# Kernel tuning notes

Hardware: AMD Instinct MI355X
Metric: run time of the kernel (lower is better)

## Reference

```python
import jax, jax.numpy as jnp
import numpy as np
from jax import lax

B, T, IN, H = 4096, 512, 11, 16


def lstm(x, Wih, Whh, bih, bhh):
    # x: [B, T, in]; PyTorch gate order i, f, g, o packed along 4H.
    xg = jnp.einsum('bti,gi->btg', x, Wih) + bih + bhh  # [B, T, 4H]
    h0 = jnp.zeros((x.shape[0], Whh.shape[1]), x.dtype)
    c0 = jnp.zeros_like(h0)

    def step(carry, xg_t):
        h, c = carry
        g = xg_t + h @ Whh.T                      # [B, 4H]
        i, f, gg, o = jnp.split(g, 4, axis=-1)
        i = jax.nn.sigmoid(i)
        f = jax.nn.sigmoid(f)
        gg = jnp.tanh(gg)
        o = jax.nn.sigmoid(o)
        c = f * c + i * gg
        h = o * jnp.tanh(c)
        return (h, c), h

    _, hs = lax.scan(step, (h0, c0), jnp.swapaxes(xg, 0, 1))  # hs: [T, B, H]
    return jnp.swapaxes(hs, 0, 1)  # [B, T, H]


def setup_inputs() -> dict:
    key = jax.random.key(0)
    ks = jax.random.split(key, 16)
    s = 1.0 / np.sqrt(H)
    u = lambda k, shape: jax.random.uniform(k, shape, jnp.float32, -s, s)
    return {
        'x': jax.random.normal(ks[0], (B, T, IN), jnp.float32),
        'Wih1': u(ks[1], (4 * H, IN)), 'Whh1': u(ks[2], (4 * H, H)),
        'bih1': u(ks[3], (4 * H,)), 'bhh1': u(ks[4], (4 * H,)),
        'Wih2': u(ks[5], (4 * H, H)), 'Whh2': u(ks[6], (4 * H, H)),
        'bih2': u(ks[7], (4 * H,)), 'bhh2': u(ks[8], (4 * H,)),
        'Wd1': u(ks[9], (8, H)), 'bd1': u(ks[10], (8,)),
        'Wd2': u(ks[11], (8, 8)), 'bd2': u(ks[12], (8,)),
        'Wd3': u(ks[13], (3, 8)), 'bd3': u(ks[14], (3,)),
    }


def reference(x, Wih1, Whh1, bih1, bhh1, Wih2, Whh2, bih2, bhh2,
              Wd1, bd1, Wd2, bd2, Wd3, bd3):
    h1 = lstm(x, Wih1, Whh1, bih1, bhh1)          # [B, T, H]
    # Dropout2d treated as identity (eval mode).
    h2 = lstm(h1, Wih2, Whh2, bih2, bhh2)          # [B, T, H]
    s = jax.nn.softmax(h2, axis=1)[:, -1, :]       # softmax over TIME, take last step -> [B, H]
    d = (s @ Wd1.T + bd1) @ Wd2.T + bd2
    d = d @ Wd3.T + bd3                            # [B, 3]
    return jax.nn.softmax(d, axis=1)
```

## Files before the change

kernel.cpp:

```cpp
#include <hip/hip_runtime.h>

#define T_STEPS 512
#define IN_DIM 11
#define ROW_PAD 12
#define H_DIM 16
#define ROW_F (T_STEPS * IN_DIM)
#define CHUNK_T 16
#define CHUNK_F (CHUNK_T * IN_DIM)
#define N_CHUNK (T_STEPS / CHUNK_T)
#define LOG2E 1.44269504088896340736f

typedef float v2f __attribute__((ext_vector_type(2)));
typedef float v4f __attribute__((ext_vector_type(4)));

__device__ __forceinline__ v2f pk_fma(v2f a, v2f b, v2f c) {
    v2f d;
    asm("v_pk_fma_f32 %0, %1, %2, %3" : "=v"(d) : "v"(a), "v"(b), "v"(c));
    return d;
}

template<int CTRL>
__device__ __forceinline__ float qperm(float v) {
    return __builtin_bit_cast(float,
        __builtin_amdgcn_update_dpp(0, __builtin_bit_cast(int, v),
                                    CTRL, 0xf, 0xf, true));
}

__device__ __forceinline__ float bcast_lane(float v, int l) {
    return __builtin_bit_cast(float,
        __builtin_amdgcn_readlane(__builtin_bit_cast(int, v), l));
}

__global__ __launch_bounds__(256, 4) void lstm2_head(
    const float* __restrict__ x,
    const float* __restrict__ Wih1, const float* __restrict__ Whh1,
    const float* __restrict__ bih1, const float* __restrict__ bhh1,
    const float* __restrict__ Wih2, const float* __restrict__ Whh2,
    const float* __restrict__ bih2, const float* __restrict__ bhh2,
    const float* __restrict__ Wd1, const float* __restrict__ bd1,
    const float* __restrict__ Wd2, const float* __restrict__ bd2,
    const float* __restrict__ Wd3, const float* __restrict__ bd3,
    float* __restrict__ out)
{
    __shared__ float xlds[4][2][212];
    __shared__ alignas(16) v2f shh[4][2][8];

    const int lane = threadIdx.x & 63;
    const int wid = __builtin_amdgcn_readfirstlane((int)(threadIdx.x >> 6));
    const int b = blockIdx.x * 4 + wid;

    const int r   = lane >> 2;
    const int gt  = lane & 3;
    const int row = gt * H_DIM + r;

    const bool is_t = (gt == 2);
    const float M   = is_t ? (-2.0f * LOG2E) : (-LOG2E);
    const float vAa = is_t ? 2.0f : 1.0f;
    const float vBc = is_t ? -1.0f : 0.0f;

    v2f wi1p[6], wh1p[8], wi2p[8], wh2p[8];
    #pragma unroll
    for (int j = 0; j < 5; ++j)
        wi1p[j] = (v2f){M * Wih1[row * IN_DIM + 2 * j], M * Wih1[row * IN_DIM + 2 * j + 1]};
    wi1p[5] = (v2f){M * Wih1[row * IN_DIM + 10], 0.0f};
    #pragma unroll
    for (int j = 0; j < 8; ++j) {
        wh1p[j] = (v2f){M * Whh1[row * H_DIM + 2 * j], M * Whh1[row * H_DIM + 2 * j + 1]};
        wi2p[j] = (v2f){M * Wih2[row * H_DIM + 2 * j], M * Wih2[row * H_DIM + 2 * j + 1]};
        wh2p[j] = (v2f){M * Whh2[row * H_DIM + 2 * j], M * Whh2[row * H_DIM + 2 * j + 1]};
    }
    const float bb1 = M * (bih1[row] + bhh1[row]);
    const float bb2 = M * (bih2[row] + bhh2[row]);
    #pragma unroll
    for (int j = 0; j < 6; ++j) asm volatile("" : "+v"(wi1p[j]));
    #pragma unroll
    for (int j = 0; j < 8; ++j) {
        asm volatile("" : "+v"(wh1p[j]));
        asm volatile("" : "+v"(wi2p[j]));
        asm volatile("" : "+v"(wh2p[j]));
    }

    const float* __restrict__ xb = x + (size_t)b * ROW_F;
    float* const xl0 = &xlds[wid][0][0];
    float* const xl1 = &xlds[wid][1][0];
    v2f* const h1mem = &shh[wid][0][0];
    v2f* const h2mem = &shh[wid][1][0];
    const v4f* const h1q4 = (const v4f*)h1mem;
    const v4f* const h2q4 = (const v4f*)h2mem;

    ((float*)h1mem)[r & 15] = 0.0f;
    ((float*)h2mem)[r & 15] = 0.0f;
    if (lane < 32) {
        const int buf = lane >> 4, rr = lane & 15;
        xlds[wid][buf][rr * ROW_PAD + IN_DIM] = 0.0f;
    }

    const int f1i = lane, f2i = lane + 64, f3i = lane + 128;
    const int p1 = (f1i / IN_DIM) * ROW_PAD + (f1i % IN_DIM);
    const int p2 = (f2i / IN_DIM) * ROW_PAD + (f2i % IN_DIM);
    const int p3 = (f3i / IN_DIM) * ROW_PAD + (f3i % IN_DIM);

    float gl0 = xb[f1i];
    float gl1 = xb[f2i];
    float gl2 = xb[min(f3i, ROW_F - 1)];

    float c1 = 0.f, c2 = 0.f, h2v = 0.f, ssum = 0.f;
    v2f h1r[8], h2r[8];
    #pragma unroll
    for (int j = 0; j < 8; ++j) { h1r[j] = (v2f){0.f, 0.f}; h2r[j] = (v2f){0.f, 0.f}; }

    for (int ck = 0; ck < N_CHUNK; ++ck) {
        float* const xbuf = (ck & 1) ? xl1 : xl0;
        xbuf[p1] = gl0;
        xbuf[p2] = gl1;
        xbuf[p3] = gl2;
        if (ck + 1 < N_CHUNK) {
            const int base = (ck + 1) * CHUNK_F;
            gl0 = xb[base + f1i];
            gl1 = xb[base + f2i];
            gl2 = xb[min(base + f3i, ROW_F - 1)];
        }

        #pragma unroll
        for (int t2 = 0; t2 < CHUNK_T; ++t2) {
            const v2f* const xr = (const v2f*)(xbuf + t2 * ROW_PAD);

            v2f a2p = pk_fma(wh2p[0], h2r[0], (v2f){bb2, 0.f});
            v2f a2q = pk_fma(wh2p[1], h2r[1], (v2f){0.f, 0.f});
            #pragma unroll
            for (int j = 2; j < 8; j += 2) {
                a2p = pk_fma(wh2p[j],     h2r[j],     a2p);
                a2q = pk_fma(wh2p[j + 1], h2r[j + 1], a2q);
            }

            v2f a1p = pk_fma(wi1p[0], xr[0], (v2f){bb1, 0.f});
            v2f a1q = pk_fma(wi1p[1], xr[1], (v2f){0.f, 0.f});
            #pragma unroll
            for (int j = 2; j < 6; j += 2) {
                a1p = pk_fma(wi1p[j],     xr[j],     a1p);
                a1q = pk_fma(wi1p[j + 1], xr[j + 1], a1q);
            }
            #pragma unroll
            for (int j = 0; j < 8; j += 2) {
                a1p = pk_fma(wh1p[j],     h1r[j],     a1p);
                a1q = pk_fma(wh1p[j + 1], h1r[j + 1], a1q);
            }

            const v2f s1 = a1p + a1q;
            const float g1 = s1.x + s1.y;
            const float a1 = __builtin_fmaf(vAa,
                __builtin_amdgcn_rcpf(1.0f + __builtin_amdgcn_exp2f(g1)), vBc);
            {
                const float gi = qperm<0x00>(a1);
                const float gf = qperm<0x55>(a1);
                const float gg = qperm<0xAA>(a1);
                const float go = qperm<0xFF>(a1);
                c1 = __builtin_fmaf(gf, c1, gi * gg);
                const float tc = __builtin_fmaf(2.0f,
                    __builtin_amdgcn_rcpf(1.0f +
                        __builtin_amdgcn_exp2f(-2.0f * LOG2E * c1)), -1.0f);
                ((float*)h1mem)[r] = go * tc;
            }
            #pragma unroll
            for (int j = 0; j < 4; ++j) {
                const v4f q = h1q4[j];
                h1r[2 * j]     = (v2f){q.x, q.y};
                h1r[2 * j + 1] = (v2f){q.z, q.w};
            }

            #pragma unroll
            for (int j = 0; j < 8; j += 2) {
                a2p = pk_fma(wi2p[j],     h1r[j],     a2p);
                a2q = pk_fma(wi2p[j + 1], h1r[j + 1], a2q);
            }

            const v2f s2 = a2p + a2q;
            const float g2 = s2.x + s2.y;
            const float a2 = __builtin_fmaf(vAa,
                __builtin_amdgcn_rcpf(1.0f + __builtin_amdgcn_exp2f(g2)), vBc);
            {
                const float gi = qperm<0x00>(a2);
                const float gf = qperm<0x55>(a2);
                const float gg = qperm<0xAA>(a2);
                const float go = qperm<0xFF>(a2);
                c2 = __builtin_fmaf(gf, c2, gi * gg);
                const float tc = __builtin_fmaf(2.0f,
                    __builtin_amdgcn_rcpf(1.0f +
                        __builtin_amdgcn_exp2f(-2.0f * LOG2E * c2)), -1.0f);
                h2v = go * tc;
                ((float*)h2mem)[r] = h2v;
            }
            #pragma unroll
            for (int j = 0; j < 4; ++j) {
                const v4f q = h2q4[j];
                h2r[2 * j]     = (v2f){q.x, q.y};
                h2r[2 * j + 1] = (v2f){q.z, q.w};
            }

            ssum += __builtin_amdgcn_exp2f(LOG2E * h2v);
        }
    }

    const float sv = __builtin_amdgcn_exp2f(LOG2E * h2v) / ssum;

    float ssb[H_DIM];
    #pragma unroll
    for (int k = 0; k < H_DIM; ++k) ssb[k] = bcast_lane(sv, 4 * k);

    const int r8 = lane & 7;
    float acc1 = bd1[r8];
    #pragma unroll
    for (int k = 0; k < H_DIM; ++k)
        acc1 = __builtin_fmaf(Wd1[r8 * H_DIM + k], ssb[k], acc1);

    float d1s[8];
    #pragma unroll
    for (int j = 0; j < 8; ++j) d1s[j] = bcast_lane(acc1, j);

    float acc2 = bd2[r8];
    #pragma unroll
    for (int k = 0; k < 8; ++k)
        acc2 = __builtin_fmaf(Wd2[r8 * 8 + k], d1s[k], acc2);

    float d2s[8];
    #pragma unroll
    for (int j = 0; j < 8; ++j) d2s[j] = bcast_lane(acc2, j);

    float lg = 0.f;
    if (lane < 3) {
        lg = bd3[lane];
        #pragma unroll
        for (int k = 0; k < 8; ++k)
            lg = __builtin_fmaf(Wd3[lane * 8 + k], d2s[k], lg);
    }
    const float l0 = bcast_lane(lg, 0);
    const float l1 = bcast_lane(lg, 1);
    const float l2 = bcast_lane(lg, 2);
    const float mx = fmaxf(l0, fmaxf(l1, l2));
    const float e0 = __builtin_amdgcn_exp2f(LOG2E * (l0 - mx));
    const float e1 = __builtin_amdgcn_exp2f(LOG2E * (l1 - mx));
    const float e2 = __builtin_amdgcn_exp2f(LOG2E * (l2 - mx));
    const float inv = 1.0f / (e0 + e1 + e2);
    if (lane < 3) {
        const float ev = (lane == 0) ? e0 : ((lane == 1) ? e1 : e2);
        out[b * 3 + lane] = ev * inv;
    }
}

extern "C" void kernel_launch(void* const* d_in, const int* in_sizes, int n_in,
                              void* d_out, int out_size, void* d_ws, size_t ws_size,
                              hipStream_t stream) {
    (void)in_sizes; (void)n_in; (void)out_size; (void)d_ws; (void)ws_size;
    const float* x    = (const float*)d_in[0];
    const float* Wih1 = (const float*)d_in[1];
    const float* Whh1 = (const float*)d_in[2];
    const float* bih1 = (const float*)d_in[3];
    const float* bhh1 = (const float*)d_in[4];
    const float* Wih2 = (const float*)d_in[5];
    const float* Whh2 = (const float*)d_in[6];
    const float* bih2 = (const float*)d_in[7];
    const float* bhh2 = (const float*)d_in[8];
    const float* Wd1  = (const float*)d_in[9];
    const float* bd1  = (const float*)d_in[10];
    const float* Wd2  = (const float*)d_in[11];
    const float* bd2  = (const float*)d_in[12];
    const float* Wd3  = (const float*)d_in[13];
    const float* bd3  = (const float*)d_in[14];

    lstm2_head<<<dim3(4096 / 4), dim3(256), 0, stream>>>(
        x, Wih1, Whh1, bih1, bhh1, Wih2, Whh2, bih2, bhh2,
        Wd1, bd1, Wd2, bd2, Wd3, bd3, (float*)d_out);
}
```

Before: 462.4 us.

## Split LSTM layers across specialized waves with a chunked h1 ring buffer

Each block now handles two sequences with four waves. Two waves run layer 1 and write h1 into a double-buffered LDS ring per 16-step chunk. The other two waves run layer 2 one chunk behind, and the waves hand off through a block barrier per chunk. This shortens each wave's per-step serial dependency chain to a single LSTM cell and doubles the number of resident waves, raising the occupancy hint to 8 blocks. The cost is a __syncthreads every chunk, one extra chunk of pipeline fill, and waves that sit idle during the first and last chunk.

Result: slower. 851.7 us (+84.2%).

```diff
diff --git a/kernel.cpp b/kernel.cpp
--- a/kernel.cpp
+++ b/kernel.cpp
@@ -31,7 +31,7 @@
         __builtin_amdgcn_readlane(__builtin_bit_cast(int, v), l));
 }
 
-__global__ __launch_bounds__(256, 4) void lstm2_head(
+__global__ __launch_bounds__(256, 8) void lstm2_head(
     const float* __restrict__ x,
     const float* __restrict__ Wih1, const float* __restrict__ Whh1,
     const float* __restrict__ bih1, const float* __restrict__ bhh1,
@@ -42,12 +42,15 @@
     const float* __restrict__ Wd3, const float* __restrict__ bd3,
     float* __restrict__ out)
 {
-    __shared__ float xlds[4][2][212];
-    __shared__ alignas(16) v2f shh[4][2][8];
+    __shared__ alignas(16) float xlds[2][212];
+    __shared__ alignas(16) float ring[2][2][CHUNK_T][H_DIM];
+    __shared__ alignas(16) float shh2[2][H_DIM];
 
     const int lane = threadIdx.x & 63;
     const int wid = __builtin_amdgcn_readfirstlane((int)(threadIdx.x >> 6));
-    const int b = blockIdx.x * 4 + wid;
+    const int isL2 = wid >> 1;
+    const int bw   = wid & 1;
+    const int b    = blockIdx.x * 2 + bw;
 
     const int r   = lane >> 2;
     const int gt  = lane & 3;
@@ -58,192 +61,205 @@
     const float vAa = is_t ? 2.0f : 1.0f;
     const float vBc = is_t ? -1.0f : 0.0f;
 
-    v2f wi1p[6], wh1p[8], wi2p[8], wh2p[8];
-    #pragma unroll
-    for (int j = 0; j < 5; ++j)
-        wi1p[j] = (v2f){M * Wih1[row * IN_DIM + 2 * j], M * Wih1[row * IN_DIM + 2 * j + 1]};
-    wi1p[5] = (v2f){M * Wih1[row * IN_DIM + 10], 0.0f};
+    v2f win[8], wrec[8];
+    float bb;
+    if (!isL2) {
+        #pragma unroll
+        for (int j = 0; j < 5; ++j)
+            win[j] = (v2f){M * Wih1[row * IN_DIM + 2 * j],
+                           M * Wih1[row * IN_DIM + 2 * j + 1]};
+        win[5] = (v2f){M * Wih1[row * IN_DIM + 10], 0.0f};
+        win[6] = (v2f){0.f, 0.f};
+        win[7] = (v2f){0.f, 0.f};
+        #pragma unroll
+        for (int j = 0; j < 8; ++j)
+            wrec[j] = (v2f){M * Whh1[row * H_DIM + 2 * j],
+                            M * Whh1[row * H_DIM + 2 * j + 1]};
+        bb = M * (bih1[row] + bhh1[row]);
+    } else {
+        #pragma unroll
+        for (int j = 0; j < 8; ++j) {
+            win[j]  = (v2f){M * Wih2[row * H_DIM + 2 * j],
+                            M * Wih2[row * H_DIM + 2 * j + 1]};
+            wrec[j] = (v2f){M * Whh2[row * H_DIM + 2 * j],
+                            M * Whh2[row * H_DIM + 2 * j + 1]};
+        }
+        bb = M * (bih2[row] + bhh2[row]);
+    }
     #pragma unroll
     for (int j = 0; j < 8; ++j) {
-        wh1p[j] = (v2f){M * Whh1[row * H_DIM + 2 * j], M * Whh1[row * H_DIM + 2 * j + 1]};
-        wi2p[j] = (v2f){M * Wih2[row * H_DIM + 2 * j], M * Wih2[row * H_DIM + 2 * j + 1]};
-        wh2p[j] = (v2f){M * Whh2[row * H_DIM + 2 * j], M * Whh2[row * H_DIM + 2 * j + 1]};
-    }
-    const float bb1 = M * (bih1[row] + bhh1[row]);
-    const float bb2 = M * (bih2[row] + bhh2[row]);
-    #pragma unroll
-    for (int j = 0; j < 6; ++j) asm volatile("" : "+v"(wi1p[j]));
-    #pragma unroll
-    for (int j = 0; j < 8; ++j) {
-        asm volatile("" : "+v"(wh1p[j]));
-        asm volatile("" : "+v"(wi2p[j]));
-        asm volatile("" : "+v"(wh2p[j]));
-    }
-
-    const float* __restrict__ xb = x + (size_t)b * ROW_F;
-    float* const xl0 = &xlds[wid][0][0];
-    float* const xl1 = &xlds[wid][1][0];
-    v2f* const h1mem = &shh[wid][0][0];
-    v2f* const h2mem = &shh[wid][1][0];
-    const v4f* const h1q4 = (const v4f*)h1mem;
-    const v4f* const h2q4 = (const v4f*)h2mem;
-
-    ((float*)h1mem)[r & 15] = 0.0f;
-    ((float*)h2mem)[r & 15] = 0.0f;
-    if (lane < 32) {
-        const int buf = lane >> 4, rr = lane & 15;
-        xlds[wid][buf][rr * ROW_PAD + IN_DIM] = 0.0f;
+        asm volatile("" : "+v"(win[j]));
+        asm volatile("" : "+v"(wrec[j]));
     }
 
     const int f1i = lane, f2i = lane + 64, f3i = lane + 128;
     const int p1 = (f1i / IN_DIM) * ROW_PAD + (f1i % IN_DIM);
     const int p2 = (f2i / IN_DIM) * ROW_PAD + (f2i % IN_DIM);
     const int p3 = (f3i / IN_DIM) * ROW_PAD + (f3i % IN_DIM);
-
-    float gl0 = xb[f1i];
-    float gl1 = xb[f2i];
-    float gl2 = xb[min(f3i, ROW_F - 1)];
-
-    float c1 = 0.f, c2 = 0.f, h2v = 0.f, ssum = 0.f;
-    v2f h1r[8], h2r[8];
+    const float* __restrict__ xb = x + (size_t)b * ROW_F;
+
+    float gl0 = 0.f, gl1 = 0.f, gl2 = 0.f;
+    if (!isL2) {
+        if (lane < 16) xlds[bw][lane * ROW_PAD + IN_DIM] = 0.0f;
+        gl0 = xb[f1i];
+        gl1 = xb[f2i];
+        gl2 = xb[min(f3i, ROW_F - 1)];
+    }
+
+    float cst = 0.f, ssum = 0.f, h2v = 0.f;
+    v2f hr[8];
     #pragma unroll
-    for (int j = 0; j < 8; ++j) { h1r[j] = (v2f){0.f, 0.f}; h2r[j] = (v2f){0.f, 0.f}; }
-
-    for (int ck = 0; ck < N_CHUNK; ++ck) {
-        float* const xbuf = (ck & 1) ? xl1 : xl0;
-        xbuf[p1] = gl0;
-        xbuf[p2] = gl1;
-        xbuf[p3] = gl2;
-        if (ck + 1 < N_CHUNK) {
-            const int base = (ck + 1) * CHUNK_F;
-            gl0 = xb[base + f1i];
-            gl1 = xb[base + f2i];
-            gl2 = xb[min(base + f3i, ROW_F - 1)];
-        }
-
-        #pragma unroll
-        for (int t2 = 0; t2 < CHUNK_T; ++t2) {
-            const v2f* const xr = (const v2f*)(xbuf + t2 * ROW_PAD);
-
-            v2f a2p = pk_fma(wh2p[0], h2r[0], (v2f){bb2, 0.f});
-            v2f a2q = pk_fma(wh2p[1], h2r[1], (v2f){0.f, 0.f});
+    for (int j = 0; j < 8; ++j) hr[j] = (v2f){0.f, 0.f};
+
+    for (int ck = 0; ck <= N_CHUNK; ++ck) {
+        __syncthreads();
+
+        if (!isL2) {
+            if (ck < N_CHUNK) {
+                float* const xbuf = &xlds[bw][0];
+                xbuf[p1] = gl0;
+                xbuf[p2] = gl1;
+                xbuf[p3] = gl2;
+                if (ck + 1 < N_CHUNK) {
+                    const int base = (ck + 1) * CHUNK_F;
+                    gl0 = xb[base + f1i];
+                    gl1 = xb[base + f2i];
+                    gl2 = xb[min(base + f3i, ROW_F - 1)];
+                }
+                float (* const rg)[H_DIM] = ring[bw][ck & 1];
+                #pragma unroll
+                for (int t2 = 0; t2 < CHUNK_T; ++t2) {
+                    const v2f* const xr = (const v2f*)(xbuf + t2 * ROW_PAD);
+                    v2f ap = pk_fma(win[0], xr[0], (v2f){bb, 0.f});
+                    v2f aq = pk_fma(win[1], xr[1], (v2f){0.f, 0.f});
+                    ap = pk_fma(win[2], xr[2], ap);
+                    aq = pk_fma(win[3], xr[3], aq);
+                    ap = pk_fma(win[4], xr[4], ap);
+                    aq = pk_fma(win[5], xr[5], aq);
+                    #pragma unroll
+                    for (int j = 0; j < 8; j += 2) {
+                        ap = pk_fma(wrec[j],     hr[j],     ap);
+                        aq = pk_fma(wrec[j + 1], hr[j + 1], aq);
+                    }
+                    const v2f s = ap + aq;
+                    const float g = s.x + s.y;
+                    const float a = __builtin_fmaf(vAa,
+                        __builtin_amdgcn_rcpf(1.0f + __builtin_amdgcn_exp2f(g)), vBc);
+                    const float gi = qperm<0x00>(a);
+                    const float gf = qperm<0x55>(a);
+                    const float gg = qperm<0xAA>(a);
+                    const float go = qperm<0xFF>(a);
+                    cst = __builtin_fmaf(gf, cst, gi * gg);
+                    const float tc = __builtin_fmaf(2.0f,
+                        __builtin_amdgcn_rcpf(1.0f +
+                            __builtin_amdgcn_exp2f(-2.0f * LOG2E * cst)), -1.0f);
+                    rg[t2][r] = go * tc;
+                    const v4f* const hq = (const v4f*)&rg[t2][0];
+                    #pragma unroll
+                    for (int j = 0; j < 4; ++j) {
+                        const v4f q = hq[j];
+                        hr[2 * j]     = (v2f){q.x, q.y};
+                        hr[2 * j + 1] = (v2f){q.z, q.w};
+                    }
+                }
+            }
+        } else {
+            if (ck >= 1) {
+                float (* const rg)[H_DIM] = ring[bw][(ck - 1) & 1];
+                #pragma unroll
+                for (int t2 = 0; t2 < CHUNK_T; ++t2) {
+                    const v4f* const hq = (const v4f*)&rg[t2][0];
+                    const v4f q0 = hq[0];
+                    const v4f q1 = hq[1];
+                    v2f ap = pk_fma(wrec[0], hr[0], (v2f){bb, 0.f});
+                    v2f aq = pk_fma(wrec[1], hr[1], (v2f){0.f, 0.f});
+                    #pragma unroll
+                    for (int j = 2; j < 8; j += 2) {
+                        ap = pk_fma(wrec[j],     hr[j],     ap);
+                        aq = pk_fma(wrec[j + 1], hr[j + 1], aq);
+                    }
+                    ap = pk_fma(win[0], (v2f){q0.x, q0.y}, ap);
+                    aq = pk_fma(win[1], (v2f){q0.z, q0.w}, aq);
+                    const v4f q2 = hq[2];
+                    const v4f q3 = hq[3];
+                    ap = pk_fma(win[2], (v2f){q1.x, q1.y}, ap);
+                    aq = pk_fma(win[3], (v2f){q1.z, q1.w}, aq);
+                    ap = pk_fma(win[4], (v2f){q2.x, q2.y}, ap);
+                    aq = pk_fma(win[5], (v2f){q2.z, q2.w}, aq);
+                    ap = pk_fma(win[6], (v2f){q3.x, q3.y}, ap);
+                    aq = pk_fma(win[7], (v2f){q3.z, q3.w}, aq);
+                    const v2f s = ap + aq;
+                    const float g = s.x + s.y;
+                    const float a = __builtin_fmaf(vAa,
+                        __builtin_amdgcn_rcpf(1.0f + __builtin_amdgcn_exp2f(g)), vBc);
+                    const float gi = qperm<0x00>(a);
+                    const float gf = qperm<0x55>(a);
+                    const float gg = qperm<0xAA>(a);
+                    const float go = qperm<0xFF>(a);
+                    cst = __builtin_fmaf(gf, cst, gi * gg);
+                    const float tc = __builtin_fmaf(2.0f,
+                        __builtin_amdgcn_rcpf(1.0f +
+                            __builtin_amdgcn_exp2f(-2.0f * LOG2E * cst)), -1.0f);
+                    h2v = go * tc;
+                    shh2[bw][r] = h2v;
+                    const v4f* const h2q = (const v4f*)&shh2[bw][0];
+                    #pragma unroll
+                    for (int j = 0; j < 4; ++j) {
+                        const v4f q = h2q[j];
+                        hr[2 * j]     = (v2f){q.x, q.y};
+                        hr[2 * j + 1] = (v2f){q.z, q.w};
+                    }
+                    ssum += __builtin_amdgcn_exp2f(LOG2E * h2v);
+                }
+            }
+        }
+    }
+
+    if (isL2) {
+        const float sv = __builtin_amdgcn_exp2f(LOG2E * h2v) / ssum;
+
+        float ssb[H_DIM];
+        #pragma unroll
+        for (int k = 0; k < H_DIM; ++k) ssb[k] = bcast_lane(sv, 4 * k);
+
+        const int r8 = lane & 7;
+        float acc1 = bd1[r8];
+        #pragma unroll
+        for (int k = 0; k < H_DIM; ++k)
+            acc1 = __builtin_fmaf(Wd1[r8 * H_DIM + k], ssb[k], acc1);
+
+        float d1s[8];
+        #pragma unroll
+        for (int j = 0; j < 8; ++j) d1s[j] = bcast_lane(acc1, j);
+
+        float acc2 = bd2[r8];
+        #pragma unroll
+        for (int k = 0; k < 8; ++k)
+            acc2 = __builtin_fmaf(Wd2[r8 * 8 + k], d1s[k], acc2);
+
+        float d2s[8];
+        #pragma unroll
+        for (int j = 0; j < 8; ++j) d2s[j] = bcast_lane(acc2, j);
+
+        float lg = 0.f;
+        if (lane < 3) {
+            lg = bd3[lane];
             #pragma unroll
-            for (int j = 2; j < 8; j += 2) {
-                a2p = pk_fma(wh2p[j],     h2r[j],     a2p);
-                a2q = pk_fma(wh2p[j + 1], h2r[j + 1], a2q);
-            }
-
-            v2f a1p = pk_fma(wi1p[0], xr[0], (v2f){bb1, 0.f});
-            v2f a1q = pk_fma(wi1p[1], xr[1], (v2f){0.f, 0.f});
-            #pragma unroll
-            for (int j = 2; j < 6; j += 2) {
-                a1p = pk_fma(wi1p[j],     xr[j],     a1p);
-                a1q = pk_fma(wi1p[j + 1], xr[j + 1], a1q);
-            }
-            #pragma unroll
-            for (int j = 0; j < 8; j += 2) {
-                a1p = pk_fma(wh1p[j],     h1r[j],     a1p);
-                a1q = pk_fma(wh1p[j + 1], h1r[j + 1], a1q);
-            }
-
-            const v2f s1 = a1p + a1q;
-            const float g1 = s1.x + s1.y;
-            const float a1 = __builtin_fmaf(vAa,
-                __builtin_amdgcn_rcpf(1.0f + __builtin_amdgcn_exp2f(g1)), vBc);
-            {
-                const float gi = qperm<0x00>(a1);
-                const float gf = qperm<0x55>(a1);
-                const float gg = qperm<0xAA>(a1);
-                const float go = qperm<0xFF>(a1);
-                c1 = __builtin_fmaf(gf, c1, gi * gg);
-                const float tc = __builtin_fmaf(2.0f,
-                    __builtin_amdgcn_rcpf(1.0f +
-                        __builtin_amdgcn_exp2f(-2.0f * LOG2E * c1)), -1.0f);
-                ((float*)h1mem)[r] = go * tc;
-            }
-            #pragma unroll
-            for (int j = 0; j < 4; ++j) {
-                const v4f q = h1q4[j];
-                h1r[2 * j]     = (v2f){q.x, q.y};
-                h1r[2 * j + 1] = (v2f){q.z, q.w};
-            }
-
-            #pragma unroll
-            for (int j = 0; j < 8; j += 2) {
-                a2p = pk_fma(wi2p[j],     h1r[j],     a2p);
-                a2q = pk_fma(wi2p[j + 1], h1r[j + 1], a2q);
-            }
-
-            const v2f s2 = a2p + a2q;
-            const float g2 = s2.x + s2.y;
-            const float a2 = __builtin_fmaf(vAa,
-                __builtin_amdgcn_rcpf(1.0f + __builtin_amdgcn_exp2f(g2)), vBc);
-            {
-                const float gi = qperm<0x00>(a2);
-                const float gf = qperm<0x55>(a2);
-                const float gg = qperm<0xAA>(a2);
-                const float go = qperm<0xFF>(a2);
-                c2 = __builtin_fmaf(gf, c2, gi * gg);
-                const float tc = __builtin_fmaf(2.0f,
-                    __builtin_amdgcn_rcpf(1.0f +
-                        __builtin_amdgcn_exp2f(-2.0f * LOG2E * c2)), -1.0f);
-                h2v = go * tc;
-                ((float*)h2mem)[r] = h2v;
-            }
-            #pragma unroll
-            for (int j = 0; j < 4; ++j) {
-                const v4f q = h2q4[j];
-                h2r[2 * j]     = (v2f){q.x, q.y};
-                h2r[2 * j + 1] = (v2f){q.z, q.w};
-            }
-
-            ssum += __builtin_amdgcn_exp2f(LOG2E * h2v);
-        }
-    }
-
-    const float sv = __builtin_amdgcn_exp2f(LOG2E * h2v) / ssum;
-
-    float ssb[H_DIM];
-    #pragma unroll
-    for (int k = 0; k < H_DIM; ++k) ssb[k] = bcast_lane(sv, 4 * k);
-
-    const int r8 = lane & 7;
-    float acc1 = bd1[r8];
-    #pragma unroll
-    for (int k = 0; k < H_DIM; ++k)
-        acc1 = __builtin_fmaf(Wd1[r8 * H_DIM + k], ssb[k], acc1);
-
-    float d1s[8];
-    #pragma unroll
-    for (int j = 0; j < 8; ++j) d1s[j] = bcast_lane(acc1, j);
-
-    float acc2 = bd2[r8];
-    #pragma unroll
-    for (int k = 0; k < 8; ++k)
-        acc2 = __builtin_fmaf(Wd2[r8 * 8 + k], d1s[k], acc2);
-
-    float d2s[8];
-    #pragma unroll
-    for (int j = 0; j < 8; ++j) d2s[j] = bcast_lane(acc2, j);
-
-    float lg = 0.f;
-    if (lane < 3) {
-        lg = bd3[lane];
-        #pragma unroll
-        for (int k = 0; k < 8; ++k)
-            lg = __builtin_fmaf(Wd3[lane * 8 + k], d2s[k], lg);
-    }
-    const float l0 = bcast_lane(lg, 0);
-    const float l1 = bcast_lane(lg, 1);
-    const float l2 = bcast_lane(lg, 2);
-    const float mx = fmaxf(l0, fmaxf(l1, l2));
-    const float e0 = __builtin_amdgcn_exp2f(LOG2E * (l0 - mx));
-    const float e1 = __builtin_amdgcn_exp2f(LOG2E * (l1 - mx));
-    const float e2 = __builtin_amdgcn_exp2f(LOG2E * (l2 - mx));
-    const float inv = 1.0f / (e0 + e1 + e2);
-    if (lane < 3) {
-        const float ev = (lane == 0) ? e0 : ((lane == 1) ? e1 : e2);
-        out[b * 3 + lane] = ev * inv;
+            for (int k = 0; k < 8; ++k)
+                lg = __builtin_fmaf(Wd3[lane * 8 + k], d2s[k], lg);
+        }
+        const float l0 = bcast_lane(lg, 0);
+        const float l1 = bcast_lane(lg, 1);
+        const float l2 = bcast_lane(lg, 2);
+        const float mx = fmaxf(l0, fmaxf(l1, l2));
+        const float e0 = __builtin_amdgcn_exp2f(LOG2E * (l0 - mx));
+        const float e1 = __builtin_amdgcn_exp2f(LOG2E * (l1 - mx));
+        const float e2 = __builtin_amdgcn_exp2f(LOG2E * (l2 - mx));
+        const float inv = 1.0f / (e0 + e1 + e2);
+        if (lane < 3) {
+            const float ev = (lane == 0) ? e0 : ((lane == 1) ? e1 : e2);
+            out[b * 3 + lane] = ev * inv;
+        }
     }
 }
 
@@ -267,7 +283,7 @@
     const float* Wd3  = (const float*)d_in[13];
     const float* bd3  = (const float*)d_in[14];
 
-    lstm2_head<<<dim3(4096 / 4), dim3(256), 0, stream>>>(
+    lstm2_head<<<dim3(4096 / 2), dim3(256), 0, stream>>>(
         x, Wih1, Whh1, bih1, bhh1, Wih2, Whh2, bih2, bhh2,
         Wd1, bd1, Wd2, bd2, Wd3, bd3, (float*)d_out);
 }
```

## Split LSTM gate matvec across quad lanes with DPP transpose-reduce

Applied to the files above, without the earlier changes.

Previously each lane computed a full 16-wide dot product (plus 11 input terms) for its own gate row and reloaded the whole hidden vector from LDS. Now each lane in a quad handles a 4-element slice of k for all four gate rows of its hidden unit. Partial sums are exchanged with quad DPP permutes, so each lane reads only a 4-float slice of h and x. This shortens the serial FMA chain and LDS read volume per step on the recurrence critical path, at the cost of extra DPP adds and a wider padded x row layout.

New measurement: 473.1 us. 2.3% more time.

```diff
diff --git a/kernel.cpp b/kernel.cpp
--- a/kernel.cpp
+++ b/kernel.cpp
@@ -2,7 +2,7 @@
 
 #define T_STEPS 512
 #define IN_DIM 11
-#define ROW_PAD 12
+#define ROW_PAD 16
 #define H_DIM 16
 #define ROW_F (T_STEPS * IN_DIM)
 #define CHUNK_T 16
@@ -30,6 +30,21 @@
     return __builtin_bit_cast(float,
         __builtin_amdgcn_readlane(__builtin_bit_cast(int, v), l));
 }
+
+#define ACT_STEP(gsum, cst, hv_out)                                           \
+    {                                                                         \
+        const float a_ = __builtin_fmaf(vAa,                                  \
+            __builtin_amdgcn_rcpf(1.0f + __builtin_amdgcn_exp2f(gsum)), vBc); \
+        const float gi_ = qperm<0x00>(a_);                                    \
+        const float gf_ = qperm<0x55>(a_);                                    \
+        const float gg_ = qperm<0xAA>(a_);                                    \
+        const float go_ = qperm<0xFF>(a_);                                    \
+        cst = __builtin_fmaf(gf_, cst, gi_ * gg_);                            \
+        const float tc_ = __builtin_fmaf(2.0f,                                \
+            __builtin_amdgcn_rcpf(1.0f +                                      \
+                __builtin_amdgcn_exp2f(-2.0f * LOG2E * cst)), -1.0f);         \
+        hv_out = go_ * tc_;                                                   \
+    }
 
 __global__ __launch_bounds__(256, 4) void lstm2_head(
     const float* __restrict__ x,
@@ -42,8 +57,8 @@
     const float* __restrict__ Wd3, const float* __restrict__ bd3,
     float* __restrict__ out)
 {
-    __shared__ float xlds[4][2][212];
-    __shared__ alignas(16) v2f shh[4][2][8];
+    __shared__ alignas(16) float xlds[4][2][CHUNK_T * ROW_PAD];
+    __shared__ alignas(16) float shh[4][2][H_DIM];
 
     const int lane = threadIdx.x & 63;
     const int wid = __builtin_amdgcn_readfirstlane((int)(threadIdx.x >> 6));
@@ -54,45 +69,52 @@
     const int row = gt * H_DIM + r;
 
     const bool is_t = (gt == 2);
-    const float M   = is_t ? (-2.0f * LOG2E) : (-LOG2E);
     const float vAa = is_t ? 2.0f : 1.0f;
     const float vBc = is_t ? -1.0f : 0.0f;
-
-    v2f wi1p[6], wh1p[8], wi2p[8], wh2p[8];
-    #pragma unroll
-    for (int j = 0; j < 5; ++j)
-        wi1p[j] = (v2f){M * Wih1[row * IN_DIM + 2 * j], M * Wih1[row * IN_DIM + 2 * j + 1]};
-    wi1p[5] = (v2f){M * Wih1[row * IN_DIM + 10], 0.0f};
-    #pragma unroll
-    for (int j = 0; j < 8; ++j) {
-        wh1p[j] = (v2f){M * Whh1[row * H_DIM + 2 * j], M * Whh1[row * H_DIM + 2 * j + 1]};
-        wi2p[j] = (v2f){M * Wih2[row * H_DIM + 2 * j], M * Wih2[row * H_DIM + 2 * j + 1]};
-        wh2p[j] = (v2f){M * Whh2[row * H_DIM + 2 * j], M * Whh2[row * H_DIM + 2 * j + 1]};
-    }
-    const float bb1 = M * (bih1[row] + bhh1[row]);
-    const float bb2 = M * (bih2[row] + bhh2[row]);
-    #pragma unroll
-    for (int j = 0; j < 6; ++j) asm volatile("" : "+v"(wi1p[j]));
-    #pragma unroll
-    for (int j = 0; j < 8; ++j) {
-        asm volatile("" : "+v"(wh1p[j]));
-        asm volatile("" : "+v"(wi2p[j]));
-        asm volatile("" : "+v"(wh2p[j]));
+    const float Mown = is_t ? (-2.0f * LOG2E) : (-LOG2E);
+
+    v2f w1h[4][2], w1x[4][2], w2h[4][2], w2i[4][2];
+    #pragma unroll
+    for (int j = 0; j < 4; ++j) {
+        const int gj = gt ^ j;
+        const float Mj = (gj == 2) ? (-2.0f * LOG2E) : (-LOG2E);
+        const int rowj = gj * H_DIM + r;
+        #pragma unroll
+        for (int i2 = 0; i2 < 2; ++i2) {
+            const int k0 = 4 * gt + 2 * i2, k1 = k0 + 1;
+            w1h[j][i2] = (v2f){Mj * Whh1[rowj * H_DIM + k0],
+                               Mj * Whh1[rowj * H_DIM + k1]};
+            w1x[j][i2] = (v2f){k0 < IN_DIM ? Mj * Wih1[rowj * IN_DIM + k0] : 0.f,
+                               k1 < IN_DIM ? Mj * Wih1[rowj * IN_DIM + k1] : 0.f};
+            w2h[j][i2] = (v2f){Mj * Whh2[rowj * H_DIM + k0],
+                               Mj * Whh2[rowj * H_DIM + k1]};
+            w2i[j][i2] = (v2f){Mj * Wih2[rowj * H_DIM + k0],
+                               Mj * Wih2[rowj * H_DIM + k1]};
+        }
+    }
+    const float bb1 = Mown * (bih1[row] + bhh1[row]);
+    const float bb2 = Mown * (bih2[row] + bhh2[row]);
+    #pragma unroll
+    for (int j = 0; j < 4; ++j) {
+        #pragma unroll
+        for (int i2 = 0; i2 < 2; ++i2) {
+            asm volatile("" : "+v"(w1h[j][i2]));
+            asm volatile("" : "+v"(w1x[j][i2]));
+            asm volatile("" : "+v"(w2h[j][i2]));
+            asm volatile("" : "+v"(w2i[j][i2]));
+        }
     }
 
     const float* __restrict__ xb = x + (size_t)b * ROW_F;
     float* const xl0 = &xlds[wid][0][0];
     float* const xl1 = &xlds[wid][1][0];
-    v2f* const h1mem = &shh[wid][0][0];
-    v2f* const h2mem = &shh[wid][1][0];
-    const v4f* const h1q4 = (const v4f*)h1mem;
-    const v4f* const h2q4 = (const v4f*)h2mem;
-
-    ((float*)h1mem)[r & 15] = 0.0f;
-    ((float*)h2mem)[r & 15] = 0.0f;
-    if (lane < 32) {
-        const int buf = lane >> 4, rr = lane & 15;
-        xlds[wid][buf][rr * ROW_PAD + IN_DIM] = 0.0f;
+    float* const hsl1 = &shh[wid][0][0];
+    float* const hsl2 = &shh[wid][1][0];
+
+    #pragma unroll
+    for (int idx = 0; idx < CHUNK_T * ROW_PAD; idx += 64) {
+        const int s = idx + lane;
+        if ((s & 15) >= IN_DIM) { xl0[s] = 0.f; xl1[s] = 0.f; }
     }
 
     const int f1i = lane, f2i = lane + 64, f3i = lane + 128;
@@ -105,9 +127,10 @@
     float gl2 = xb[min(f3i, ROW_F - 1)];
 
     float c1 = 0.f, c2 = 0.f, h2v = 0.f, ssum = 0.f;
-    v2f h1r[8], h2r[8];
-    #pragma unroll
-    for (int j = 0; j < 8; ++j) { h1r[j] = (v2f){0.f, 0.f}; h2r[j] = (v2f){0.f, 0.f}; }
+    v2f h1a = (v2f){0.f, 0.f}, h1b = (v2f){0.f, 0.f};
+    v2f h2a = (v2f){0.f, 0.f}, h2b = (v2f){0.f, 0.f};
+
+    const int xoff = 4 * gt;
 
     for (int ck = 0; ck < N_CHUNK; ++ck) {
         float* const xbuf = (ck & 1) ? xl1 : xl0;
@@ -123,79 +146,68 @@
 
         #pragma unroll
         for (int t2 = 0; t2 < CHUNK_T; ++t2) {
-            const v2f* const xr = (const v2f*)(xbuf + t2 * ROW_PAD);
-
-            v2f a2p = pk_fma(wh2p[0], h2r[0], (v2f){bb2, 0.f});
-            v2f a2q = pk_fma(wh2p[1], h2r[1], (v2f){0.f, 0.f});
-            #pragma unroll
-            for (int j = 2; j < 8; j += 2) {
-                a2p = pk_fma(wh2p[j],     h2r[j],     a2p);
-                a2q = pk_fma(wh2p[j + 1], h2r[j + 1], a2q);
-            }
-
-            v2f a1p = pk_fma(wi1p[0], xr[0], (v2f){bb1, 0.f});
-            v2f a1q = pk_fma(wi1p[1], xr[1], (v2f){0.f, 0.f});
-            #pragma unroll
-            for (int j = 2; j < 6; j += 2) {
-                a1p = pk_fma(wi1p[j],     xr[j],     a1p);
-                a1q = pk_fma(wi1p[j + 1], xr[j + 1], a1q);
-            }
-            #pragma unroll
-            for (int j = 0; j < 8; j += 2) {
-                a1p = pk_fma(wh1p[j],     h1r[j],     a1p);
-                a1q = pk_fma(wh1p[j + 1], h1r[j + 1], a1q);
-            }
-
-            const v2f s1 = a1p + a1q;
-            const float g1 = s1.x + s1.y;
-            const float a1 = __builtin_fmaf(vAa,
-                __builtin_amdgcn_rcpf(1.0f + __builtin_amdgcn_exp2f(g1)), vBc);
-            {
-                const float gi = qperm<0x00>(a1);
-                const float gf = qperm<0x55>(a1);
-                const float gg = qperm<0xAA>(a1);
-                const float go = qperm<0xFF>(a1);
-                c1 = __builtin_fmaf(gf, c1, gi * gg);
-                const float tc = __builtin_fmaf(2.0f,
-                    __builtin_amdgcn_rcpf(1.0f +
-                        __builtin_amdgcn_exp2f(-2.0f * LOG2E * c1)), -1.0f);
-                ((float*)h1mem)[r] = go * tc;
-            }
-            #pragma unroll
-            for (int j = 0; j < 4; ++j) {
-                const v4f q = h1q4[j];
-                h1r[2 * j]     = (v2f){q.x, q.y};
-                h1r[2 * j + 1] = (v2f){q.z, q.w};
-            }
-
-            #pragma unroll
-            for (int j = 0; j < 8; j += 2) {
-                a2p = pk_fma(wi2p[j],     h1r[j],     a2p);
-                a2q = pk_fma(wi2p[j + 1], h1r[j + 1], a2q);
-            }
-
-            const v2f s2 = a2p + a2q;
-            const float g2 = s2.x + s2.y;
-            const float a2 = __builtin_fmaf(vAa,
-                __builtin_amdgcn_rcpf(1.0f + __builtin_amdgcn_exp2f(g2)), vBc);
-            {
-                const float gi = qperm<0x00>(a2);
-                const float gf = qperm<0x55>(a2);
-                const float gg = qperm<0xAA>(a2);
-                const float go = qperm<0xFF>(a2);
-                c2 = __builtin_fmaf(gf, c2, gi * gg);
-                const float tc = __builtin_fmaf(2.0f,
-                    __builtin_amdgcn_rcpf(1.0f +
-                        __builtin_amdgcn_exp2f(-2.0f * LOG2E * c2)), -1.0f);
-                h2v = go * tc;
-                ((float*)h2mem)[r] = h2v;
-            }
-            #pragma unroll
-            for (int j = 0; j < 4; ++j) {
-                const v4f q = h2q4[j];
-                h2r[2 * j]     = (v2f){q.x, q.y};
-                h2r[2 * j + 1] = (v2f){q.z, q.w};
-            }
+            const v4f xq = *(const v4f*)(xbuf + t2 * ROW_PAD + xoff);
+            const v2f x01 = (v2f){xq.x, xq.y};
+            const v2f x23 = (v2f){xq.z, xq.w};
+
+            v2f d0 = pk_fma(w1h[0][0], h1a, (v2f){bb1, 0.f});
+            d0 = pk_fma(w1h[0][1], h1b, d0);
+            d0 = pk_fma(w1x[0][0], x01, d0);
+            d0 = pk_fma(w1x[0][1], x23, d0);
+            v2f d1 = pk_fma(w1h[1][0], h1a, (v2f){0.f, 0.f});
+            d1 = pk_fma(w1h[1][1], h1b, d1);
+            d1 = pk_fma(w1x[1][0], x01, d1);
+            d1 = pk_fma(w1x[1][1], x23, d1);
+            v2f d2 = pk_fma(w1h[2][0], h1a, (v2f){0.f, 0.f});
+            d2 = pk_fma(w1h[2][1], h1b, d2);
+            d2 = pk_fma(w1x[2][0], x01, d2);
+            d2 = pk_fma(w1x[2][1], x23, d2);
+            v2f d3 = pk_fma(w1h[3][0], h1a, (v2f){0.f, 0.f});
+            d3 = pk_fma(w1h[3][1], h1b, d3);
+            d3 = pk_fma(w1x[3][0], x01, d3);
+            d3 = pk_fma(w1x[3][1], x23, d3);
+            const float u0 = d0.x + d0.y;
+            const float u1 = d1.x + d1.y;
+            const float u2 = d2.x + d2.y;
+            const float u3 = d3.x + d3.y;
+            const float g1v = u0 + qperm<0xB1>(u1)
+                                 + qperm<0x4E>(u2) + qperm<0x1B>(u3);
+
+            float h1v;
+            ACT_STEP(g1v, c1, h1v);
+            hsl1[r] = h1v;
+            const v4f h1q = *(const v4f*)(hsl1 + xoff);
+            h1a = (v2f){h1q.x, h1q.y};
+            h1b = (v2f){h1q.z, h1q.w};
+
+            v2f e0 = pk_fma(w2h[0][0], h2a, (v2f){bb2, 0.f});
+            e0 = pk_fma(w2h[0][1], h2b, e0);
+            e0 = pk_fma(w2i[0][0], h1a, e0);
+            e0 = pk_fma(w2i[0][1], h1b, e0);
+            v2f e1 = pk_fma(w2h[1][0], h2a, (v2f){0.f, 0.f});
+            e1 = pk_fma(w2h[1][1], h2b, e1);
+            e1 = pk_fma(w2i[1][0], h1a, e1);
+            e1 = pk_fma(w2i[1][1], h1b, e1);
+            v2f e2 = pk_fma(w2h[2][0], h2a, (v2f){0.f, 0.f});
+            e2 = pk_fma(w2h[2][1], h2b, e2);
+            e2 = pk_fma(w2i[2][0], h1a, e2);
+            e2 = pk_fma(w2i[2][1], h1b, e2);
+            v2f e3 = pk_fma(w2h[3][0], h2a, (v2f){0.f, 0.f});
+            e3 = pk_fma(w2h[3][1], h2b, e3);
+            e3 = pk_fma(w2i[3][0], h1a, e3);
+            e3 = pk_fma(w2i[3][1], h1b, e3);
+            const float v0 = e0.x + e0.y;
+            const float v1 = e1.x + e1.y;
+            const float v2 = e2.x + e2.y;
+            const float v3 = e3.x + e3.y;
+            const float g2v = v0 + qperm<0xB1>(v1)
+                                 + qperm<0x4E>(v2) + qperm<0x1B>(v3);
+
+            ACT_STEP(g2v, c2, h2v);
+            hsl2[r] = h2v;
+            const v4f h2q = *(const v4f*)(hsl2 + xoff);
+            h2a = (v2f){h2q.x, h2q.y};
+            h2b = (v2f){h2q.z, h2q.w};
 
             ssum += __builtin_amdgcn_exp2f(LOG2E * h2v);
         }
```

## Read x directly from global per step instead of staging chunks through LDS

Applied to the files above, without the earlier changes.

Removes the double-buffered LDS staging of input chunks and the chunk loop. Each timestep now loads its 11 input values straight from global memory (a uniform per-wave address, so effectively scalar or broadcast loads), computes the input projection with scalar FMAs, and folds it into the packed recurrent accumulator. The goal is to drop the LDS writes and reads and the chunk bookkeeping from the serial recurrence. The cost is global or cache load latency inside the dependent loop, which now relies on unroll-by-8 to hide it.

Measured after the change: 505.7 us. 1.09x slower.

```diff
diff --git a/kernel.cpp b/kernel.cpp
--- a/kernel.cpp
+++ b/kernel.cpp
@@ -2,12 +2,8 @@
 
 #define T_STEPS 512
 #define IN_DIM 11
-#define ROW_PAD 12
 #define H_DIM 16
 #define ROW_F (T_STEPS * IN_DIM)
-#define CHUNK_T 16
-#define CHUNK_F (CHUNK_T * IN_DIM)
-#define N_CHUNK (T_STEPS / CHUNK_T)
 #define LOG2E 1.44269504088896340736f
 
 typedef float v2f __attribute__((ext_vector_type(2)));
@@ -30,6 +26,21 @@
     return __builtin_bit_cast(float,
         __builtin_amdgcn_readlane(__builtin_bit_cast(int, v), l));
 }
+
+#define ACT_STEP(gsum, cst, hv_out)                                           \
+    {                                                                         \
+        const float a_ = __builtin_fmaf(vAa,                                  \
+            __builtin_amdgcn_rcpf(1.0f + __builtin_amdgcn_exp2f(gsum)), vBc); \
+        const float gi_ = qperm<0x00>(a_);                                    \
+        const float gf_ = qperm<0x55>(a_);                                    \
+        const float gg_ = qperm<0xAA>(a_);                                    \
+        const float go_ = qperm<0xFF>(a_);                                    \
+        cst = __builtin_fmaf(gf_, cst, gi_ * gg_);                            \
+        const float tc_ = __builtin_fmaf(2.0f,                                \
+            __builtin_amdgcn_rcpf(1.0f +                                      \
+                __builtin_amdgcn_exp2f(-2.0f * LOG2E * cst)), -1.0f);         \
+        hv_out = go_ * tc_;                                                   \
+    }
 
 __global__ __launch_bounds__(256, 4) void lstm2_head(
     const float* __restrict__ x,
@@ -42,8 +53,7 @@
     const float* __restrict__ Wd3, const float* __restrict__ bd3,
     float* __restrict__ out)
 {
-    __shared__ float xlds[4][2][212];
-    __shared__ alignas(16) v2f shh[4][2][8];
+    __shared__ alignas(16) float shh[4][2][H_DIM];
 
     const int lane = threadIdx.x & 63;
     const int wid = __builtin_amdgcn_readfirstlane((int)(threadIdx.x >> 6));
@@ -58,11 +68,10 @@
     const float vAa = is_t ? 2.0f : 1.0f;
     const float vBc = is_t ? -1.0f : 0.0f;
 
-    v2f wi1p[6], wh1p[8], wi2p[8], wh2p[8];
-    #pragma unroll
-    for (int j = 0; j < 5; ++j)
-        wi1p[j] = (v2f){M * Wih1[row * IN_DIM + 2 * j], M * Wih1[row * IN_DIM + 2 * j + 1]};
-    wi1p[5] = (v2f){M * Wih1[row * IN_DIM + 10], 0.0f};
+    float wx[IN_DIM];
+    #pragma unroll
+    for (int k = 0; k < IN_DIM; ++k) wx[k] = M * Wih1[row * IN_DIM + k];
+    v2f wh1p[8], wi2p[8], wh2p[8];
     #pragma unroll
     for (int j = 0; j < 8; ++j) {
         wh1p[j] = (v2f){M * Whh1[row * H_DIM + 2 * j], M * Whh1[row * H_DIM + 2 * j + 1]};
@@ -72,7 +81,7 @@
     const float bb1 = M * (bih1[row] + bhh1[row]);
     const float bb2 = M * (bih2[row] + bhh2[row]);
     #pragma unroll
-    for (int j = 0; j < 6; ++j) asm volatile("" : "+v"(wi1p[j]));
+    for (int k = 0; k < IN_DIM; ++k) asm volatile("" : "+v"(wx[k]));
     #pragma unroll
     for (int j = 0; j < 8; ++j) {
         asm volatile("" : "+v"(wh1p[j]));
@@ -80,125 +89,82 @@
         asm volatile("" : "+v"(wh2p[j]));
     }
 
+    float* const hs1 = &shh[wid][0][0];
+    float* const hs2 = &shh[wid][1][0];
+    const v4f* const h1q4 = (const v4f*)hs1;
+    const v4f* const h2q4 = (const v4f*)hs2;
+    hs1[r] = 0.0f;
+    hs2[r] = 0.0f;
+
     const float* __restrict__ xb = x + (size_t)b * ROW_F;
-    float* const xl0 = &xlds[wid][0][0];
-    float* const xl1 = &xlds[wid][1][0];
-    v2f* const h1mem = &shh[wid][0][0];
-    v2f* const h2mem = &shh[wid][1][0];
-    const v4f* const h1q4 = (const v4f*)h1mem;
-    const v4f* const h2q4 = (const v4f*)h2mem;
-
-    ((float*)h1mem)[r & 15] = 0.0f;
-    ((float*)h2mem)[r & 15] = 0.0f;
-    if (lane < 32) {
-        const int buf = lane >> 4, rr = lane & 15;
-        xlds[wid][buf][rr * ROW_PAD + IN_DIM] = 0.0f;
-    }
-
-    const int f1i = lane, f2i = lane + 64, f3i = lane + 128;
-    const int p1 = (f1i / IN_DIM) * ROW_PAD + (f1i % IN_DIM);
-    const int p2 = (f2i / IN_DIM) * ROW_PAD + (f2i % IN_DIM);
-    const int p3 = (f3i / IN_DIM) * ROW_PAD + (f3i % IN_DIM);
-
-    float gl0 = xb[f1i];
-    float gl1 = xb[f2i];
-    float gl2 = xb[min(f3i, ROW_F - 1)];
 
     float c1 = 0.f, c2 = 0.f, h2v = 0.f, ssum = 0.f;
     v2f h1r[8], h2r[8];
     #pragma unroll
     for (int j = 0; j < 8; ++j) { h1r[j] = (v2f){0.f, 0.f}; h2r[j] = (v2f){0.f, 0.f}; }
 
-    for (int ck = 0; ck < N_CHUNK; ++ck) {
-        float* const xbuf = (ck & 1) ? xl1 : xl0;
-        xbuf[p1] = gl0;
-        xbuf[p2] = gl1;
-        xbuf[p3] = gl2;
-        if (ck + 1 < N_CHUNK) {
-            const int base = (ck + 1) * CHUNK_F;
-            gl0 = xb[base + f1i];
-            gl1 = xb[base + f2i];
-            gl2 = xb[min(base + f3i, ROW_F - 1)];
-        }
-
-        #pragma unroll
-        for (int t2 = 0; t2 < CHUNK_T; ++t2) {
-            const v2f* const xr = (const v2f*)(xbuf + t2 * ROW_PAD);
-
-            v2f a2p = pk_fma(wh2p[0], h2r[0], (v2f){bb2, 0.f});
-            v2f a2q = pk_fma(wh2p[1], h2r[1], (v2f){0.f, 0.f});
-            #pragma unroll
-            for (int j = 2; j < 8; j += 2) {
-                a2p = pk_fma(wh2p[j],     h2r[j],     a2p);
-                a2q = pk_fma(wh2p[j + 1], h2r[j + 1], a2q);
-            }
-
-            v2f a1p = pk_fma(wi1p[0], xr[0], (v2f){bb1, 0.f});
-            v2f a1q = pk_fma(wi1p[1], xr[1], (v2f){0.f, 0.f});
-            #pragma unroll
-            for (int j = 2; j < 6; j += 2) {
-                a1p = pk_fma(wi1p[j],     xr[j],     a1p);
-                a1q = pk_fma(wi1p[j + 1], xr[j + 1], a1q);
-            }
-            #pragma unroll
-            for (int j = 0; j < 8; j += 2) {
-                a1p = pk_fma(wh1p[j],     h1r[j],     a1p);
-                a1q = pk_fma(wh1p[j + 1], h1r[j + 1], a1q);
-            }
-
-            const v2f s1 = a1p + a1q;
-            const float g1 = s1.x + s1.y;
-            const float a1 = __builtin_fmaf(vAa,
-                __builtin_amdgcn_rcpf(1.0f + __builtin_amdgcn_exp2f(g1)), vBc);
-            {
-                const float gi = qperm<0x00>(a1);
-                const float gf = qperm<0x55>(a1);
-                const float gg = qperm<0xAA>(a1);
-                const float go = qperm<0xFF>(a1);
-                c1 = __builtin_fmaf(gf, c1, gi * gg);
-                const float tc = __builtin_fmaf(2.0f,
-                    __builtin_amdgcn_rcpf(1.0f +
-                        __builtin_amdgcn_exp2f(-2.0f * LOG2E * c1)), -1.0f);
-                ((float*)h1mem)[r] = go * tc;
-            }
-            #pragma unroll
-            for (int j = 0; j < 4; ++j) {
-                const v4f q = h1q4[j];
-                h1r[2 * j]     = (v2f){q.x, q.y};
-                h1r[2 * j + 1] = (v2f){q.z, q.w};
-            }
-
-            #pragma unroll
-            for (int j = 0; j < 8; j += 2) {
-                a2p = pk_fma(wi2p[j],     h1r[j],     a2p);
-                a2q = pk_fma(wi2p[j + 1], h1r[j + 1], a2q);
-            }
-
-            const v2f s2 = a2p + a2q;
-            const float g2 = s2.x + s2.y;
-            const float a2 = __builtin_fmaf(vAa,
-                __builtin_amdgcn_rcpf(1.0f + __builtin_amdgcn_exp2f(g2)), vBc);
-            {
-                const float gi = qperm<0x00>(a2);
-                const float gf = qperm<0x55>(a2);
-                const float gg = qperm<0xAA>(a2);
-                const float go = qperm<0xFF>(a2);
-                c2 = __builtin_fmaf(gf, c2, gi * gg);
-                const float tc = __builtin_fmaf(2.0f,
-                    __builtin_amdgcn_rcpf(1.0f +
-                        __builtin_amdgcn_exp2f(-2.0f * LOG2E * c2)), -1.0f);
-                h2v = go * tc;
-                ((float*)h2mem)[r] = h2v;
-            }
-            #pragma unroll
-            for (int j = 0; j < 4; ++j) {
-                const v4f q = h2q4[j];
-                h2r[2 * j]     = (v2f){q.x, q.y};
-                h2r[2 * j + 1] = (v2f){q.z, q.w};
-            }
-
-            ssum += __builtin_amdgcn_exp2f(LOG2E * h2v);
-        }
+    #pragma unroll 8
+    for (int t = 0; t < T_STEPS; ++t) {
+        const float* __restrict__ xr = xb + t * IN_DIM;
+
+        float xs0 = __builtin_fmaf(wx[0], xr[0], bb1);
+        float xs1 = wx[1] * xr[1];
+        xs0 = __builtin_fmaf(wx[2], xr[2], xs0);
+        xs1 = __builtin_fmaf(wx[3], xr[3], xs1);
+        xs0 = __builtin_fmaf(wx[4], xr[4], xs0);
+        xs1 = __builtin_fmaf(wx[5], xr[5], xs1);
+        xs0 = __builtin_fmaf(wx[6], xr[6], xs0);
+        xs1 = __builtin_fmaf(wx[7], xr[7], xs1);
+        xs0 = __builtin_fmaf(wx[8], xr[8], xs0);
+        xs1 = __builtin_fmaf(wx[9], xr[9], xs1);
+        xs0 = __builtin_fmaf(wx[10], xr[10], xs0);
+
+        v2f a2p = pk_fma(wh2p[0], h2r[0], (v2f){bb2, 0.f});
+        v2f a2q = pk_fma(wh2p[1], h2r[1], (v2f){0.f, 0.f});
+        #pragma unroll
+        for (int j = 2; j < 8; j += 2) {
+            a2p = pk_fma(wh2p[j],     h2r[j],     a2p);
+            a2q = pk_fma(wh2p[j + 1], h2r[j + 1], a2q);
+        }
+
+        v2f a1p = pk_fma(wh1p[0], h1r[0], (v2f){xs0, xs1});
+        v2f a1q = pk_fma(wh1p[1], h1r[1], (v2f){0.f, 0.f});
+        #pragma unroll
+        for (int j = 2; j < 8; j += 2) {
+            a1p = pk_fma(wh1p[j],     h1r[j],     a1p);
+            a1q = pk_fma(wh1p[j + 1], h1r[j + 1], a1q);
+        }
+
+        const v2f s1 = a1p + a1q;
+        const float g1 = s1.x + s1.y;
+        float h1v;
+        ACT_STEP(g1, c1, h1v);
+        hs1[r] = h1v;
+        #pragma unroll
+        for (int j = 0; j < 4; ++j) {
+            const v4f q = h1q4[j];
+            h1r[2 * j]     = (v2f){q.x, q.y};
+            h1r[2 * j + 1] = (v2f){q.z, q.w};
+        }
+
+        #pragma unroll
+        for (int j = 0; j < 8; j += 2) {
+            a2p = pk_fma(wi2p[j],     h1r[j],     a2p);
+            a2q = pk_fma(wi2p[j + 1], h1r[j + 1], a2q);
+        }
+
+        const v2f s2 = a2p + a2q;
+        const float g2 = s2.x + s2.y;
+        ACT_STEP(g2, c2, h2v);
+        hs2[r] = h2v;
+        #pragma unroll
+        for (int j = 0; j < 4; ++j) {
+            const v4f q = h2q4[j];
+            h2r[2 * j]     = (v2f){q.x, q.y};
+            h2r[2 * j + 1] = (v2f){q.z, q.w};
+        }
+
+        ssum += __builtin_amdgcn_exp2f(LOG2E * h2v);
     }
 
     const float sv = __builtin_amdgcn_exp2f(LOG2E * h2v) / ssum;
```
